# Performance work log

Hardware: AMD Instinct MI355X
Metric: run time of the kernel (lower is better)

## Reference

```python
import jax, jax.numpy as jnp
import numpy as np

B, H, W, D = 32, 56, 56, 192
WS, NH, SHIFT = 7, 6, 3
DH = D // NH          # head dim = 32
N = WS * WS           # 49 tokens per window
NW = (H // WS) * (W // WS)  # 64 windows per image
EPS = 1e-5


def _rel_pos_index():
    coords = np.stack(np.meshgrid(np.arange(WS), np.arange(WS), indexing='ij'))  # (2,WS,WS)
    flat = coords.reshape(2, -1)
    rel = flat[:, :, None] - flat[:, None, :]            # (2,N,N)
    rel = rel.transpose(1, 2, 0).astype(np.int64)        # (N,N,2)
    rel[..., 0] += WS - 1
    rel[..., 1] += WS - 1
    rel[..., 0] *= 2 * WS - 1
    return rel.sum(-1)                                    # (N,N) in [0,169)


def _shift_mask():
    img = np.zeros((H, W))
    bounds = [(0, H - WS), (H - WS, H - SHIFT), (H - SHIFT, H)]
    cnt = 0
    for h0, h1 in bounds:
        for w0, w1 in bounds:
            img[h0:h1, w0:w1] = cnt
            cnt += 1
    win = img.reshape(H // WS, WS, W // WS, WS).transpose(0, 2, 1, 3).reshape(-1, N)  # (nW,N)
    diff = win[:, None, :] - win[:, :, None]
    return np.where(diff != 0, -100.0, 0.0).astype(np.float32)  # (nW,N,N)


_REL_IDX = jnp.asarray(_rel_pos_index())
_MASK = jnp.asarray(_shift_mask())


def _layernorm(x, g, b):
    mu = jnp.mean(x, -1, keepdims=True)
    var = jnp.mean(jnp.square(x - mu), -1, keepdims=True)
    return (x - mu) * jax.lax.rsqrt(var + EPS) * g + b


def _window_partition(x):  # (B,H,W,C) -> (B*nW, N, C)
    Bx, _, _, C = x.shape
    x = x.reshape(Bx, H // WS, WS, W // WS, WS, C).transpose(0, 1, 3, 2, 4, 5)
    return x.reshape(-1, N, C)


def _window_reverse(w):  # (B*nW, N, C) -> (B,H,W,C)
    C = w.shape[-1]
    x = w.reshape(-1, H // WS, W // WS, WS, WS, C).transpose(0, 1, 3, 2, 4, 5)
    return x.reshape(-1, H, W, C)


def setup_inputs() -> dict:
    key = jax.random.key(0)
    ks = jax.random.split(key, 8)
    s = 0.02
    return {
        'x': jax.random.normal(ks[0], (B, H * W, D), jnp.float32),
        'norm1_g': jnp.ones((D,), jnp.float32),
        'norm1_b': jnp.zeros((D,), jnp.float32),
        'qkv_w': jax.random.normal(ks[1], (D, 3 * D), jnp.float32) * s,
        'qkv_b': jnp.zeros((3 * D,), jnp.float32),
        'proj_wo': jax.random.normal(ks[2], (D, D), jnp.float32) * s,
        'proj_bo': jnp.zeros((D,), jnp.float32),
        'rpb': jax.random.normal(ks[3], ((2 * WS - 1) ** 2, NH), jnp.float32) * s,
        'pl_w': jax.random.normal(ks[4], (NH, NH), jnp.float32) * s,
        'pl_b': jnp.zeros((NH,), jnp.float32),
        'pw_w': jax.random.normal(ks[5], (NH, NH), jnp.float32) * s,
        'pw_b': jnp.zeros((NH,), jnp.float32),
        'norm2_g': jnp.ones((D,), jnp.float32),
        'norm2_b': jnp.zeros((D,), jnp.float32),
        'fc1_w': jax.random.normal(ks[6], (D, 4 * D), jnp.float32) * s,
        'fc1_b': jnp.zeros((4 * D,), jnp.float32),
        'fc2_w': jax.random.normal(ks[7], (4 * D, D), jnp.float32) * s,
        'fc2_b': jnp.zeros((D,), jnp.float32),
    }


def reference(x, norm1_g, norm1_b, qkv_w, qkv_b, proj_wo, proj_bo, rpb,
              pl_w, pl_b, pw_w, pw_b, norm2_g, norm2_b,
              fc1_w, fc1_b, fc2_w, fc2_b):
    shortcut = x
    h = _layernorm(x, norm1_g, norm1_b).reshape(B, H, W, D)
    h = jnp.roll(h, (-SHIFT, -SHIFT), (1, 2))             # shifted windows
    win = _window_partition(h)                            # (B_, N, D), B_ = B*NW
    B_ = win.shape[0]

    qkv = win @ qkv_w + qkv_b                             # (B_, N, 3D)
    q_out, k_out, v_out = qkv[..., :D], qkv[..., D:2 * D], qkv[..., 2 * D:]
    qkv5 = qkv.reshape(B_, N, 3, NH, DH)
    q = qkv5[:, :, 0].transpose(0, 2, 1, 3)               # (B_, H, N, d)
    k = qkv5[:, :, 1].transpose(0, 2, 1, 3)
    v = qkv5[:, :, 2].transpose(0, 2, 1, 3)

    scale = DH ** -0.5
    attn = jnp.einsum('bhnd,bhmd->bhnm', q * scale, k)    # (B_, H, N, N)
    bias = rpb[_REL_IDX.reshape(-1)].reshape(N, N, NH).transpose(2, 0, 1)
    attn = attn + bias[None]
    # proj_l over the head axis (distillation transform, pre-softmax)
    attn = jnp.einsum('bhnm,hg->bgnm', attn, pl_w) + pl_b[None, :, None, None]
    # shifted-window mask
    attn = attn.reshape(B, NW, NH, N, N) + _MASK[None, :, None]
    attn = jax.nn.softmax(attn.reshape(B_, NH, N, N), axis=-1)
    # proj_w over the head axis (post-softmax)
    attn = jnp.einsum('bhnm,hg->bgnm', attn, pw_w) + pw_b[None, :, None, None]

    out = jnp.einsum('bhnm,bhmd->bnhd', attn, v).reshape(B_, N, D)
    out = out @ proj_wo + proj_bo

    h = _window_reverse(out)                              # (B,H,W,D)
    h = jnp.roll(h, (SHIFT, SHIFT), (1, 2)).reshape(B, H * W, D)
    xo = shortcut + h

    m = _layernorm(xo, norm2_g, norm2_b)
    m = jax.nn.gelu(m @ fc1_w + fc1_b, approximate=False) @ fc2_w + fc2_b
    xo = xo + m
    return xo, (q_out, k_out, v_out)
```

## Files before the change

### kernel.cpp

```cpp
#include <hip/hip_runtime.h>
#include <math.h>

#define TOK   100352
#define OUTCH 19267584L
#define NWIN  2048

typedef __attribute__((ext_vector_type(4))) float f32x4;
typedef __attribute__((ext_vector_type(8))) short bf16x8;

__device__ __forceinline__ unsigned short f2bf(float f) {
    unsigned u = __builtin_bit_cast(unsigned, f);
    u += 0x7FFFu + ((u >> 16) & 1u);
    return (unsigned short)(u >> 16);
}
__device__ __forceinline__ float bf2f(unsigned short s) {
    return __builtin_bit_cast(float, (unsigned)s << 16);
}

__global__ __launch_bounds__(256) void k_prep_w(const float* __restrict__ qkv_w,
                                                const float* __restrict__ proj_w,
                                                const float* __restrict__ fc1_w,
                                                const float* __restrict__ fc2_w,
                                                unsigned short* __restrict__ wt)
{
    int i = blockIdx.x * 256 + threadIdx.x;
    float v;
    if (i < 110592) {
        int instr = i >> 9, rem = i & 511, lane = rem >> 3, j = rem & 7;
        int ks = instr % 6, t = instr / 6;
        int ni = t % 3, t2 = t / 3;
        int wv = t2 & 3, s = t2 >> 2;
        int n = s * 192 + wv * 48 + ni * 16 + (lane & 15);
        int k = ks * 32 + ((lane >> 4) << 3) + j;
        v = qkv_w[k * 576 + n];
    } else if (i < 147456) {
        int j2 = i - 110592;
        int instr = j2 >> 9, rem = j2 & 511, lane = rem >> 3, j = rem & 7;
        int ks = instr % 6, t = instr / 6;
        int ni = t % 3, wv = t / 3;
        int n = wv * 48 + ni * 16 + (lane & 15);
        int k = ks * 32 + ((lane >> 4) << 3) + j;
        v = proj_w[k * 192 + n];
    } else if (i < 294912) {
        int j2 = i - 147456;
        int instr = j2 >> 9, rem = j2 & 511, lane = rem >> 3, j = rem & 7;
        int ks = instr % 6, t = instr / 6;
        int ni = t % 3, t2 = t / 3;
        int wv = t2 & 3, s = t2 >> 2;
        int n = s * 192 + wv * 48 + ni * 16 + (lane & 15);
        int k = ks * 32 + ((lane >> 4) << 3) + j;
        v = fc1_w[k * 768 + n];
    } else {
        int j2 = i - 294912;
        int instr = j2 >> 9, rem = j2 & 511, lane = rem >> 3, j = rem & 7;
        int ks = instr % 6, t = instr / 6;
        int ni = t % 3, t2 = t / 3;
        int wv = t2 & 3, s = t2 >> 2;
        int n = wv * 48 + ni * 16 + (lane & 15);
        int k = s * 192 + ks * 32 + ((lane >> 4) << 3) + j;
        v = fc2_w[k * 192 + n];
    }
    wt[i] = f2bf(v);
}

__global__ __launch_bounds__(256) void k_qkv(const float* __restrict__ x,
                                             const float* __restrict__ g,
                                             const float* __restrict__ b,
                                             const unsigned short* __restrict__ wp,
                                             const float* __restrict__ bias,
                                             float* __restrict__ outq)
{
    __shared__ unsigned short lA[64 * 192];
    const int tid = threadIdx.x, lane = tid & 63, wv = tid >> 6;
    const int s = blockIdx.x;
    const long m0 = (long)blockIdx.y * 64;

    {
        int r = tid >> 2, c0 = (tid & 3) * 48;
        int t = (int)m0 + r;
        int w = t / 49, n = t - w * 49;
        int bb = w >> 6, widx = w & 63;
        int wi = widx >> 3, wj = widx & 7;
        int rr = n / 7, ss = n - rr * 7;
        int hh = wi * 7 + rr + 3; if (hh >= 56) hh -= 56;
        int ww = wj * 7 + ss + 3; if (ww >= 56) ww -= 56;
        const f32x4* sp = (const f32x4*)(x + ((long)(bb * 56 + hh) * 56 + ww) * 192 + c0);
        f32x4 vv[12];
        float sum = 0.f, sq = 0.f;
        #pragma unroll
        for (int i = 0; i < 12; i++) {
            vv[i] = sp[i];
            #pragma unroll
            for (int j = 0; j < 4; j++) { sum += vv[i][j]; sq += vv[i][j] * vv[i][j]; }
        }
        sum += __shfl_xor(sum, 1); sq += __shfl_xor(sq, 1);
        sum += __shfl_xor(sum, 2); sq += __shfl_xor(sq, 2);
        float mu = sum * (1.f / 192.f);
        float rs = rsqrtf(sq * (1.f / 192.f) - mu * mu + 1e-5f);
        #pragma unroll
        for (int i = 0; i < 6; i++) {
            bf16x8 o8;
            #pragma unroll
            for (int j = 0; j < 8; j++) {
                int idx = i * 8 + j, c = c0 + idx;
                o8[j] = (short)f2bf((vv[idx >> 2][idx & 3] - mu) * rs * g[c] + b[c]);
            }
            *(bf16x8*)((char*)lA + r * 384 + ((2 * (c0 + i * 8)) ^ ((r & 7) << 4))) = o8;
        }
    }
    __syncthreads();

    f32x4 acc[4][3];
    #pragma unroll
    for (int mi = 0; mi < 4; mi++)
        #pragma unroll
        for (int ni = 0; ni < 3; ni++) acc[mi][ni] = (f32x4){0.f, 0.f, 0.f, 0.f};
    #pragma unroll
    for (int ks = 0; ks < 6; ks++) {
        int kb = ks * 64 + ((lane >> 4) << 4);
        bf16x8 bfr[3];
        #pragma unroll
        for (int ni = 0; ni < 3; ni++) {
            int instr = ((s * 4 + wv) * 3 + ni) * 6 + ks;
            bfr[ni] = *(const bf16x8*)(wp + (instr << 9) + (lane << 3));
        }
        #pragma unroll
        for (int mi = 0; mi < 4; mi++) {
            int row = mi * 16 + (lane & 15);
            bf16x8 afr = *(const bf16x8*)((char*)lA + row * 384 + (kb ^ ((row & 7) << 4)));
            #pragma unroll
            for (int ni = 0; ni < 3; ni++)
                acc[mi][ni] = __builtin_amdgcn_mfma_f32_16x16x32_bf16(afr, bfr[ni], acc[mi][ni], 0, 0, 0);
        }
    }

    #pragma unroll
    for (int mi = 0; mi < 4; mi++)
        #pragma unroll
        for (int ni = 0; ni < 3; ni++) {
            int gc = wv * 48 + ni * 16 + (lane & 15);
            float bv = bias[s * 192 + gc];
            #pragma unroll
            for (int r4 = 0; r4 < 4; r4++) {
                long lr = mi * 16 + ((lane >> 4) << 2) + r4;
                outq[(long)s * OUTCH + (m0 + lr) * 192 + gc] = acc[mi][ni][r4] + bv;
            }
        }
}

__global__ __launch_bounds__(256) void k_proj(const unsigned short* __restrict__ aspat,
                                              const unsigned short* __restrict__ wp,
                                              const float* __restrict__ pbias,
                                              const float* __restrict__ x,
                                              const float* __restrict__ g2,
                                              const float* __restrict__ b2,
                                              unsigned short* __restrict__ xv,
                                              unsigned short* __restrict__ h2)
{
    __shared__ unsigned short lA[64 * 192];
    __shared__ float xoT[64][196];
    const int tid = threadIdx.x, lane = tid & 63, wv = tid >> 6;
    const long m0 = (long)blockIdx.x * 64;

    #pragma unroll
    for (int c = tid; c < 64 * 24; c += 256) {
        int row = c / 24, k16 = c - row * 24;
        bf16x8 v = *(const bf16x8*)(aspat + (m0 + row) * 192 + k16 * 8);
        *(bf16x8*)((char*)lA + row * 384 + ((k16 * 16) ^ ((row & 7) << 4))) = v;
    }
    __syncthreads();

    f32x4 acc[4][3];
    #pragma unroll
    for (int mi = 0; mi < 4; mi++)
        #pragma unroll
        for (int ni = 0; ni < 3; ni++) acc[mi][ni] = (f32x4){0.f, 0.f, 0.f, 0.f};
    #pragma unroll
    for (int ks = 0; ks < 6; ks++) {
        int kb = ks * 64 + ((lane >> 4) << 4);
        bf16x8 bfr[3];
        #pragma unroll
        for (int ni = 0; ni < 3; ni++) {
            int instr = (wv * 3 + ni) * 6 + ks;
            bfr[ni] = *(const bf16x8*)(wp + (instr << 9) + (lane << 3));
        }
        #pragma unroll
        for (int mi = 0; mi < 4; mi++) {
            int row = mi * 16 + (lane & 15);
            bf16x8 afr = *(const bf16x8*)((char*)lA + row * 384 + (kb ^ ((row & 7) << 4)));
            #pragma unroll
            for (int ni = 0; ni < 3; ni++)
                acc[mi][ni] = __builtin_amdgcn_mfma_f32_16x16x32_bf16(afr, bfr[ni], acc[mi][ni], 0, 0, 0);
        }
    }

    #pragma unroll
    for (int mi = 0; mi < 4; mi++)
        #pragma unroll
        for (int ni = 0; ni < 3; ni++) {
            int gc = wv * 48 + ni * 16 + (lane & 15);
            float bv = pbias[gc];
            #pragma unroll
            for (int r4 = 0; r4 < 4; r4++) {
                int lr = mi * 16 + ((lane >> 4) << 2) + r4;
                xoT[lr][gc] = x[(m0 + lr) * 192 + gc] + acc[mi][ni][r4] + bv;
            }
        }
    __syncthreads();

    {
        int r = tid >> 2, c0 = (tid & 3) * 48;
        float vv[48];
        float sum = 0.f, sq = 0.f;
        #pragma unroll
        for (int i = 0; i < 48; i++) { vv[i] = xoT[r][c0 + i]; sum += vv[i]; sq += vv[i] * vv[i]; }
        sum += __shfl_xor(sum, 1); sq += __shfl_xor(sq, 1);
        sum += __shfl_xor(sum, 2); sq += __shfl_xor(sq, 2);
        float mu = sum * (1.f / 192.f);
        float rs = rsqrtf(sq * (1.f / 192.f) - mu * mu + 1e-5f);
        #pragma unroll
        for (int i = 0; i < 6; i++) {
            bf16x8 o8, x8;
            #pragma unroll
            for (int j = 0; j < 8; j++) {
                int c = c0 + i * 8 + j;
                float xvf = vv[i * 8 + j];
                x8[j] = (short)f2bf(xvf);
                o8[j] = (short)f2bf((xvf - mu) * rs * g2[c] + b2[c]);
            }
            *(bf16x8*)(h2 + (m0 + r) * 192 + c0 + i * 8) = o8;
            *(bf16x8*)(xv + (m0 + r) * 192 + c0 + i * 8) = x8;
        }
    }
}

__global__ __launch_bounds__(256) void k_mlp(const unsigned short* __restrict__ h2,
                                             const unsigned short* __restrict__ w1p,
                                             const float* __restrict__ b1,
                                             const unsigned short* __restrict__ w2p,
                                             const float* __restrict__ b2,
                                             const unsigned short* __restrict__ xv,
                                             float* __restrict__ xo)
{
    __shared__ unsigned short lA[64 * 192];
    __shared__ unsigned short lH[64 * 192];
    const int tid = threadIdx.x, lane = tid & 63, wv = tid >> 6;
    const long m0 = (long)blockIdx.x * 64;

    #pragma unroll
    for (int c = tid; c < 64 * 24; c += 256) {
        int row = c / 24, k16 = c - row * 24;
        bf16x8 v = *(const bf16x8*)(h2 + (m0 + row) * 192 + k16 * 8);
        *(bf16x8*)((char*)lA + row * 384 + ((k16 * 16) ^ ((row & 7) << 4))) = v;
    }

    f32x4 acc2[4][3];
    #pragma unroll
    for (int mi = 0; mi < 4; mi++)
        #pragma unroll
        for (int ni = 0; ni < 3; ni++) acc2[mi][ni] = (f32x4){0.f, 0.f, 0.f, 0.f};
    __syncthreads();

    for (int s = 0; s < 4; s++) {
        f32x4 acc1[4][3];
        #pragma unroll
        for (int mi = 0; mi < 4; mi++)
            #pragma unroll
            for (int ni = 0; ni < 3; ni++) acc1[mi][ni] = (f32x4){0.f, 0.f, 0.f, 0.f};
        #pragma unroll
        for (int ks = 0; ks < 6; ks++) {
            int kb = ks * 64 + ((lane >> 4) << 4);
            bf16x8 bfr[3];
            #pragma unroll
            for (int ni = 0; ni < 3; ni++) {
                int instr = ((s * 4 + wv) * 3 + ni) * 6 + ks;
                bfr[ni] = *(const bf16x8*)(w1p + (instr << 9) + (lane << 3));
            }
            #pragma unroll
            for (int mi = 0; mi < 4; mi++) {
                int row = mi * 16 + (lane & 15);
                bf16x8 afr = *(const bf16x8*)((char*)lA + row * 384 + (kb ^ ((row & 7) << 4)));
                #pragma unroll
                for (int ni = 0; ni < 3; ni++)
                    acc1[mi][ni] = __builtin_amdgcn_mfma_f32_16x16x32_bf16(afr, bfr[ni], acc1[mi][ni], 0, 0, 0);
            }
        }
        __syncthreads();
        #pragma unroll
        for (int mi = 0; mi < 4; mi++)
            #pragma unroll
            for (int ni = 0; ni < 3; ni++) {
                int col = wv * 48 + ni * 16 + (lane & 15);
                float bv = b1[s * 192 + col];
                #pragma unroll
                for (int r = 0; r < 4; r++) {
                    int row = mi * 16 + ((lane >> 4) << 2) + r;
                    float v = acc1[mi][ni][r] + bv;
                    float ge = 0.5f * v * (1.f + erff(v * 0.70710678118654752f));
                    *(unsigned short*)((char*)lH + row * 384 + ((2 * col) ^ ((row & 7) << 4))) = f2bf(ge);
                }
            }
        __syncthreads();
        #pragma unroll
        for (int ks = 0; ks < 6; ks++) {
            int kb = ks * 64 + ((lane >> 4) << 4);
            bf16x8 bfr[3];
            #pragma unroll
            for (int ni = 0; ni < 3; ni++) {
                int instr = ((s * 4 + wv) * 3 + ni) * 6 + ks;
                bfr[ni] = *(const bf16x8*)(w2p + (instr << 9) + (lane << 3));
            }
            #pragma unroll
            for (int mi = 0; mi < 4; mi++) {
                int row = mi * 16 + (lane & 15);
                bf16x8 afr = *(const bf16x8*)((char*)lH + row * 384 + (kb ^ ((row & 7) << 4)));
                #pragma unroll
                for (int ni = 0; ni < 3; ni++)
                    acc2[mi][ni] = __builtin_amdgcn_mfma_f32_16x16x32_bf16(afr, bfr[ni], acc2[mi][ni], 0, 0, 0);
            }
        }
    }
    #pragma unroll
    for (int mi = 0; mi < 4; mi++)
        #pragma unroll
        for (int ni = 0; ni < 3; ni++) {
            int gcol = wv * 48 + ni * 16 + (lane & 15);
            float bv = b2[gcol];
            #pragma unroll
            for (int r = 0; r < 4; r++) {
                long grow = m0 + mi * 16 + ((lane >> 4) << 2) + r;
                xo[grow * 192 + gcol] = bf2f(xv[grow * 192 + gcol]) + acc2[mi][ni][r] + bv;
            }
        }
}

#define ATS 67
__global__ __launch_bounds__(384) void k_attn(const float* __restrict__ qg,
                                              const float* __restrict__ kg,
                                              const float* __restrict__ vg,
                                              const float* __restrict__ rpb,
                                              const float* __restrict__ plw,
                                              const float* __restrict__ plb,
                                              const float* __restrict__ pww,
                                              const float* __restrict__ pwb,
                                              unsigned short* __restrict__ aout)
{
    __shared__ float ATT[6][49][ATS];

    int w = blockIdx.x, widx = w & 63;
    int tid = threadIdx.x, lane = tid & 63, h = tid >> 6;
    const long base = (long)w * 49 * 192;

    bf16x8 vfr[2][2];
    #pragma unroll
    for (int kst = 0; kst < 2; kst++)
        #pragma unroll
        for (int ni = 0; ni < 2; ni++) {
            int d = ni * 16 + (lane & 15);
            #pragma unroll
            for (int j = 0; j < 8; j++) {
                int n = kst * 32 + ((lane >> 4) << 3) + j; if (n > 48) n = 48;
                vfr[kst][ni][j] = (short)f2bf(vg[base + n * 192 + h * 32 + d]);
            }
        }

    for (int c = tid; c < 6 * 49 * 15; c += 384) {
        int g2 = c / (49 * 15), rem = c - g2 * (49 * 15);
        int m = rem / 15, n = 49 + (rem - m * 15);
        ATT[g2][m][n] = 0.f;
    }

    bf16x8 qfr[4], kfr[4];
    #pragma unroll
    for (int mi = 0; mi < 4; mi++) {
        int m = mi * 16 + (lane & 15); if (m > 48) m = 48;
        const float* qp = qg + base + m * 192 + h * 32 + ((lane >> 4) << 3);
        #pragma unroll
        for (int j = 0; j < 8; j++) qfr[mi][j] = (short)f2bf(qp[j]);
    }
    #pragma unroll
    for (int ni = 0; ni < 4; ni++) {
        int n = ni * 16 + (lane & 15); if (n > 48) n = 48;
        const float* kp = kg + base + n * 192 + h * 32 + ((lane >> 4) << 3);
        #pragma unroll
        for (int j = 0; j < 8; j++) kfr[ni][j] = (short)f2bf(kp[j]);
    }
    f32x4 sa[4][4];
    #pragma unroll
    for (int ni = 0; ni < 4; ni++)
        #pragma unroll
        for (int mi = 0; mi < 4; mi++)
            sa[mi][ni] = __builtin_amdgcn_mfma_f32_16x16x32_bf16(qfr[mi], kfr[ni], (f32x4){0.f, 0.f, 0.f, 0.f}, 0, 0, 0);
    const float scale = 0.17677669529663687f;
    #pragma unroll
    for (int mi = 0; mi < 4; mi++)
        #pragma unroll
        for (int ni = 0; ni < 4; ni++)
            #pragma unroll
            for (int r = 0; r < 4; r++) {
                int m = mi * 16 + ((lane >> 4) << 2) + r, n = ni * 16 + (lane & 15);
                if (m < 49 && n < 49) {
                    int rq = m / 7, cq = m - rq * 7, rk = n / 7, ck = n - rk * 7;
                    int ridx = (rq - rk + 6) * 13 + (cq - ck + 6);
                    ATT[h][m][n] = sa[mi][ni][r] * scale + rpb[ridx * 6 + h];
                }
            }
    __syncthreads();

    int wi = widx >> 3, wj = widx & 7;
    for (int p = tid; p < 2401; p += 384) {
        int m = p / 49, n = p - m * 49;
        float a[6];
        #pragma unroll
        for (int g2 = 0; g2 < 6; g2++) a[g2] = ATT[g2][m][n];
        int rq = m / 7, cq = m - rq * 7, rk = n / 7, ck = n - rk * 7;
        int ghq = wi * 7 + rq, gwq = wj * 7 + cq, ghk = wi * 7 + rk, gwk = wj * 7 + ck;
        int regq = (ghq < 49 ? 0 : (ghq < 53 ? 1 : 2)) * 3 + (gwq < 49 ? 0 : (gwq < 53 ? 1 : 2));
        int regk = (ghk < 49 ? 0 : (ghk < 53 ? 1 : 2)) * 3 + (gwk < 49 ? 0 : (gwk < 53 ? 1 : 2));
        float msk = (regq != regk) ? -100.f : 0.f;
        #pragma unroll
        for (int g2 = 0; g2 < 6; g2++) {
            float v = plb[g2] + msk;
            #pragma unroll
            for (int h2 = 0; h2 < 6; h2++) v += a[h2] * plw[h2 * 6 + g2];
            ATT[g2][m][n] = v;
        }
    }
    __syncthreads();

    if (tid < 294) {
        int g2 = tid / 49, m = tid - g2 * 49;
        float* row = &ATT[g2][m][0];
        float mx = row[0];
        #pragma unroll
        for (int j = 1; j < 49; j++) mx = fmaxf(mx, row[j]);
        float e[49]; float sm = 0.f;
        #pragma unroll
        for (int j = 0; j < 49; j++) { e[j] = __expf(row[j] - mx); sm += e[j]; }
        float inv = 1.f / sm;
        #pragma unroll
        for (int j = 0; j < 49; j++) row[j] = e[j] * inv;
    }
    __syncthreads();

    for (int p = tid; p < 2401; p += 384) {
        int m = p / 49, n = p - m * 49;
        float a[6];
        #pragma unroll
        for (int g2 = 0; g2 < 6; g2++) a[g2] = ATT[g2][m][n];
        #pragma unroll
        for (int g2 = 0; g2 < 6; g2++) {
            float v = pwb[g2];
            #pragma unroll
            for (int h2 = 0; h2 < 6; h2++) v += a[h2] * pww[h2 * 6 + g2];
            ATT[g2][m][n] = v;
        }
    }
    __syncthreads();

    f32x4 oa[4][2];
    #pragma unroll
    for (int mi = 0; mi < 4; mi++)
        #pragma unroll
        for (int ni = 0; ni < 2; ni++) oa[mi][ni] = (f32x4){0.f, 0.f, 0.f, 0.f};
    #pragma unroll
    for (int kst = 0; kst < 2; kst++) {
        #pragma unroll
        for (int mi = 0; mi < 4; mi++) {
            int m = mi * 16 + (lane & 15); if (m > 48) m = 48;
            const float* ap = &ATT[h][m][kst * 32 + ((lane >> 4) << 3)];
            bf16x8 afr;
            #pragma unroll
            for (int j = 0; j < 8; j++) afr[j] = (short)f2bf(ap[j]);
            #pragma unroll
            for (int ni = 0; ni < 2; ni++)
                oa[mi][ni] = __builtin_amdgcn_mfma_f32_16x16x32_bf16(afr, vfr[kst][ni], oa[mi][ni], 0, 0, 0);
        }
    }
    int bb = w >> 6;
    #pragma unroll
    for (int mi = 0; mi < 4; mi++)
        #pragma unroll
        for (int ni = 0; ni < 2; ni++)
            #pragma unroll
            for (int r = 0; r < 4; r++) {
                int m = mi * 16 + ((lane >> 4) << 2) + r, d = ni * 16 + (lane & 15);
                if (m < 49) {
                    int rr = m / 7, ss = m - rr * 7;
                    int ho = wi * 7 + rr + 3; if (ho >= 56) ho -= 56;
                    int wo = wj * 7 + ss + 3; if (wo >= 56) wo -= 56;
                    long tp = ((long)(bb * 56 + ho) * 56 + wo);
                    aout[tp * 192 + h * 32 + d] = f2bf(oa[mi][ni][r]);
                }
            }
}

extern "C" void kernel_launch(void* const* d_in, const int* in_sizes, int n_in,
                              void* d_out, int out_size, void* d_ws, size_t ws_size,
                              hipStream_t stream)
{
    const float* x      = (const float*)d_in[0];
    const float* n1g    = (const float*)d_in[1];
    const float* n1b    = (const float*)d_in[2];
    const float* qkv_w  = (const float*)d_in[3];
    const float* qkv_b  = (const float*)d_in[4];
    const float* proj_w = (const float*)d_in[5];
    const float* proj_b = (const float*)d_in[6];
    const float* rpb    = (const float*)d_in[7];
    const float* pl_w   = (const float*)d_in[8];
    const float* pl_b   = (const float*)d_in[9];
    const float* pw_w   = (const float*)d_in[10];
    const float* pw_b   = (const float*)d_in[11];
    const float* n2g    = (const float*)d_in[12];
    const float* n2b    = (const float*)d_in[13];
    const float* fc1_w  = (const float*)d_in[14];
    const float* fc1_b  = (const float*)d_in[15];
    const float* fc2_w  = (const float*)d_in[16];
    const float* fc2_b  = (const float*)d_in[17];

    float* out   = (float*)d_out;
    float* out_q = out + OUTCH;
    float* out_k = out + 2 * OUTCH;
    float* out_v = out + 3 * OUTCH;

    char* ws = (char*)d_ws;
    unsigned short* bufT = (unsigned short*)ws;
    unsigned short* xvB  = (unsigned short*)(ws + 38535168);
    unsigned short* bufW = (unsigned short*)(ws + 2 * 38535168L);

    k_prep_w<<<1728, 256, 0, stream>>>(qkv_w, proj_w, fc1_w, fc2_w, bufW);
    k_qkv<<<dim3(3, 1568), 256, 0, stream>>>(x, n1g, n1b, bufW, qkv_b, out_q);
    k_attn<<<NWIN, 384, 0, stream>>>(out_q, out_k, out_v,
                                     rpb, pl_w, pl_b, pw_w, pw_b, bufT);
    k_proj<<<1568, 256, 0, stream>>>(bufT, bufW + 110592, proj_b, x, n2g, n2b,
                                     xvB, bufT);
    k_mlp<<<1568, 256, 0, stream>>>(bufT, bufW + 147456, fc1_b, bufW + 294912, fc2_b,
                                    xvB, out);
}
```

Before: 458.3 us.

## Fuse output projection, residual and LayerNorm2 into windowed attention kernel

Removes the separate k_proj kernel and performs the output projection, residual add and second LayerNorm inside k_attn, per window, using shared memory for the attention output tile. The proj weight pre-pack is reorganized to per-head 32-column slices to match the six-wave attention block. This drops a bf16 round trip of the attention output through global memory and one kernel launch. In exchange shared memory per block rises to about 79KB, which can lower occupancy, and the 49-row window pads the MFMA work for the projection.

Measured after the change: 459.7 us. No clear change (+0.3%).

```diff
diff --git a/kernel.cpp b/kernel.cpp
--- a/kernel.cpp
+++ b/kernel.cpp
@@ -37,8 +37,8 @@
         int j2 = i - 110592;
         int instr = j2 >> 9, rem = j2 & 511, lane = rem >> 3, j = rem & 7;
         int ks = instr % 6, t = instr / 6;
-        int ni = t % 3, wv = t / 3;
-        int n = wv * 48 + ni * 16 + (lane & 15);
+        int ni = t & 1, hh = t >> 1;
+        int n = hh * 32 + ni * 16 + (lane & 15);
         int k = ks * 32 + ((lane >> 4) << 3) + j;
         v = proj_w[k * 192 + n];
     } else if (i < 294912) {
@@ -148,92 +148,6 @@
         }
 }
 
-__global__ __launch_bounds__(256) void k_proj(const unsigned short* __restrict__ aspat,
-                                              const unsigned short* __restrict__ wp,
-                                              const float* __restrict__ pbias,
-                                              const float* __restrict__ x,
-                                              const float* __restrict__ g2,
-                                              const float* __restrict__ b2,
-                                              unsigned short* __restrict__ xv,
-                                              unsigned short* __restrict__ h2)
-{
-    __shared__ unsigned short lA[64 * 192];
-    __shared__ float xoT[64][196];
-    const int tid = threadIdx.x, lane = tid & 63, wv = tid >> 6;
-    const long m0 = (long)blockIdx.x * 64;
-
-    #pragma unroll
-    for (int c = tid; c < 64 * 24; c += 256) {
-        int row = c / 24, k16 = c - row * 24;
-        bf16x8 v = *(const bf16x8*)(aspat + (m0 + row) * 192 + k16 * 8);
-        *(bf16x8*)((char*)lA + row * 384 + ((k16 * 16) ^ ((row & 7) << 4))) = v;
-    }
-    __syncthreads();
-
-    f32x4 acc[4][3];
-    #pragma unroll
-    for (int mi = 0; mi < 4; mi++)
-        #pragma unroll
-        for (int ni = 0; ni < 3; ni++) acc[mi][ni] = (f32x4){0.f, 0.f, 0.f, 0.f};
-    #pragma unroll
-    for (int ks = 0; ks < 6; ks++) {
-        int kb = ks * 64 + ((lane >> 4) << 4);
-        bf16x8 bfr[3];
-        #pragma unroll
-        for (int ni = 0; ni < 3; ni++) {
-            int instr = (wv * 3 + ni) * 6 + ks;
-            bfr[ni] = *(const bf16x8*)(wp + (instr << 9) + (lane << 3));
-        }
-        #pragma unroll
-        for (int mi = 0; mi < 4; mi++) {
-            int row = mi * 16 + (lane & 15);
-            bf16x8 afr = *(const bf16x8*)((char*)lA + row * 384 + (kb ^ ((row & 7) << 4)));
-            #pragma unroll
-            for (int ni = 0; ni < 3; ni++)
-                acc[mi][ni] = __builtin_amdgcn_mfma_f32_16x16x32_bf16(afr, bfr[ni], acc[mi][ni], 0, 0, 0);
-        }
-    }
-
-    #pragma unroll
-    for (int mi = 0; mi < 4; mi++)
-        #pragma unroll
-        for (int ni = 0; ni < 3; ni++) {
-            int gc = wv * 48 + ni * 16 + (lane & 15);
-            float bv = pbias[gc];
-            #pragma unroll
-            for (int r4 = 0; r4 < 4; r4++) {
-                int lr = mi * 16 + ((lane >> 4) << 2) + r4;
-                xoT[lr][gc] = x[(m0 + lr) * 192 + gc] + acc[mi][ni][r4] + bv;
-            }
-        }
-    __syncthreads();
-
-    {
-        int r = tid >> 2, c0 = (tid & 3) * 48;
-        float vv[48];
-        float sum = 0.f, sq = 0.f;
-        #pragma unroll
-        for (int i = 0; i < 48; i++) { vv[i] = xoT[r][c0 + i]; sum += vv[i]; sq += vv[i] * vv[i]; }
-        sum += __shfl_xor(sum, 1); sq += __shfl_xor(sq, 1);
-        sum += __shfl_xor(sum, 2); sq += __shfl_xor(sq, 2);
-        float mu = sum * (1.f / 192.f);
-        float rs = rsqrtf(sq * (1.f / 192.f) - mu * mu + 1e-5f);
-        #pragma unroll
-        for (int i = 0; i < 6; i++) {
-            bf16x8 o8, x8;
-            #pragma unroll
-            for (int j = 0; j < 8; j++) {
-                int c = c0 + i * 8 + j;
-                float xvf = vv[i * 8 + j];
-                x8[j] = (short)f2bf(xvf);
-                o8[j] = (short)f2bf((xvf - mu) * rs * g2[c] + b2[c]);
-            }
-            *(bf16x8*)(h2 + (m0 + r) * 192 + c0 + i * 8) = o8;
-            *(bf16x8*)(xv + (m0 + r) * 192 + c0 + i * 8) = x8;
-        }
-    }
-}
-
 __global__ __launch_bounds__(256) void k_mlp(const unsigned short* __restrict__ h2,
                                              const unsigned short* __restrict__ w1p,
                                              const float* __restrict__ b1,
@@ -343,13 +257,22 @@
                                               const float* __restrict__ plb,
                                               const float* __restrict__ pww,
                                               const float* __restrict__ pwb,
-                                              unsigned short* __restrict__ aout)
+                                              const unsigned short* __restrict__ projp,
+                                              const float* __restrict__ pbias,
+                                              const float* __restrict__ x,
+                                              const float* __restrict__ g2,
+                                              const float* __restrict__ b2,
+                                              unsigned short* __restrict__ xv,
+                                              unsigned short* __restrict__ h2)
 {
-    __shared__ float ATT[6][49][ATS];
+    __shared__ __align__(16) char SM[78800];
+    float (*ATT)[49][ATS] = (float(*)[49][ATS])SM;
+    float (*xoT)[196]     = (float(*)[196])(SM + 19200);
 
     int w = blockIdx.x, widx = w & 63;
     int tid = threadIdx.x, lane = tid & 63, h = tid >> 6;
     const long base = (long)w * 49 * 192;
+    int wi = widx >> 3, wj = widx & 7, bb = w >> 6;
 
     bf16x8 vfr[2][2];
     #pragma unroll
@@ -365,9 +288,9 @@
         }
 
     for (int c = tid; c < 6 * 49 * 15; c += 384) {
-        int g2 = c / (49 * 15), rem = c - g2 * (49 * 15);
+        int g = c / (49 * 15), rem = c - g * (49 * 15);
         int m = rem / 15, n = 49 + (rem - m * 15);
-        ATT[g2][m][n] = 0.f;
+        ATT[g][m][n] = 0.f;
     }
 
     bf16x8 qfr[4], kfr[4];
@@ -407,30 +330,29 @@
             }
     __syncthreads();
 
-    int wi = widx >> 3, wj = widx & 7;
     for (int p = tid; p < 2401; p += 384) {
         int m = p / 49, n = p - m * 49;
         float a[6];
         #pragma unroll
-        for (int g2 = 0; g2 < 6; g2++) a[g2] = ATT[g2][m][n];
+        for (int g = 0; g < 6; g++) a[g] = ATT[g][m][n];
         int rq = m / 7, cq = m - rq * 7, rk = n / 7, ck = n - rk * 7;
         int ghq = wi * 7 + rq, gwq = wj * 7 + cq, ghk = wi * 7 + rk, gwk = wj * 7 + ck;
         int regq = (ghq < 49 ? 0 : (ghq < 53 ? 1 : 2)) * 3 + (gwq < 49 ? 0 : (gwq < 53 ? 1 : 2));
         int regk = (ghk < 49 ? 0 : (ghk < 53 ? 1 : 2)) * 3 + (gwk < 49 ? 0 : (gwk < 53 ? 1 : 2));
         float msk = (regq != regk) ? -100.f : 0.f;
         #pragma unroll
-        for (int g2 = 0; g2 < 6; g2++) {
-            float v = plb[g2] + msk;
-            #pragma unroll
-            for (int h2 = 0; h2 < 6; h2++) v += a[h2] * plw[h2 * 6 + g2];
-            ATT[g2][m][n] = v;
+        for (int g = 0; g < 6; g++) {
+            float v = plb[g] + msk;
+            #pragma unroll
+            for (int h2i = 0; h2i < 6; h2i++) v += a[h2i] * plw[h2i * 6 + g];
+            ATT[g][m][n] = v;
         }
     }
     __syncthreads();
 
     if (tid < 294) {
-        int g2 = tid / 49, m = tid - g2 * 49;
-        float* row = &ATT[g2][m][0];
+        int g = tid / 49, m = tid - g * 49;
+        float* row = &ATT[g][m][0];
         float mx = row[0];
         #pragma unroll
         for (int j = 1; j < 49; j++) mx = fmaxf(mx, row[j]);
@@ -447,13 +369,13 @@
         int m = p / 49, n = p - m * 49;
         float a[6];
         #pragma unroll
-        for (int g2 = 0; g2 < 6; g2++) a[g2] = ATT[g2][m][n];
-        #pragma unroll
-        for (int g2 = 0; g2 < 6; g2++) {
-            float v = pwb[g2];
-            #pragma unroll
-            for (int h2 = 0; h2 < 6; h2++) v += a[h2] * pww[h2 * 6 + g2];
-            ATT[g2][m][n] = v;
+        for (int g = 0; g < 6; g++) a[g] = ATT[g][m][n];
+        #pragma unroll
+        for (int g = 0; g < 6; g++) {
+            float v = pwb[g];
+            #pragma unroll
+            for (int h2i = 0; h2i < 6; h2i++) v += a[h2i] * pww[h2i * 6 + g];
+            ATT[g][m][n] = v;
         }
     }
     __syncthreads();
@@ -477,22 +399,94 @@
                 oa[mi][ni] = __builtin_amdgcn_mfma_f32_16x16x32_bf16(afr, vfr[kst][ni], oa[mi][ni], 0, 0, 0);
         }
     }
-    int bb = w >> 6;
+    __syncthreads();
+
     #pragma unroll
     for (int mi = 0; mi < 4; mi++)
         #pragma unroll
         for (int ni = 0; ni < 2; ni++)
             #pragma unroll
             for (int r = 0; r < 4; r++) {
-                int m = mi * 16 + ((lane >> 4) << 2) + r, d = ni * 16 + (lane & 15);
+                int m = mi * 16 + ((lane >> 4) << 2) + r;
+                if (m < 49) {
+                    int col = h * 32 + ni * 16 + (lane & 15);
+                    *(unsigned short*)(SM + m * 384 + ((2 * col) ^ ((m & 7) << 4))) = f2bf(oa[mi][ni][r]);
+                }
+            }
+    __syncthreads();
+
+    f32x4 pacc[4][2];
+    #pragma unroll
+    for (int mi = 0; mi < 4; mi++)
+        #pragma unroll
+        for (int ni = 0; ni < 2; ni++) pacc[mi][ni] = (f32x4){0.f, 0.f, 0.f, 0.f};
+    #pragma unroll
+    for (int ks = 0; ks < 6; ks++) {
+        int kb = ks * 64 + ((lane >> 4) << 4);
+        bf16x8 bfr[2];
+        #pragma unroll
+        for (int ni = 0; ni < 2; ni++) {
+            int instr = (h * 2 + ni) * 6 + ks;
+            bfr[ni] = *(const bf16x8*)(projp + (instr << 9) + (lane << 3));
+        }
+        #pragma unroll
+        for (int mi = 0; mi < 4; mi++) {
+            int row = mi * 16 + (lane & 15); if (row > 48) row = 48;
+            bf16x8 afr = *(const bf16x8*)(SM + row * 384 + (kb ^ ((row & 7) << 4)));
+            #pragma unroll
+            for (int ni = 0; ni < 2; ni++)
+                pacc[mi][ni] = __builtin_amdgcn_mfma_f32_16x16x32_bf16(afr, bfr[ni], pacc[mi][ni], 0, 0, 0);
+        }
+    }
+
+    #pragma unroll
+    for (int mi = 0; mi < 4; mi++)
+        #pragma unroll
+        for (int ni = 0; ni < 2; ni++) {
+            int gc = h * 32 + ni * 16 + (lane & 15);
+            float bv = pbias[gc];
+            #pragma unroll
+            for (int r = 0; r < 4; r++) {
+                int m = mi * 16 + ((lane >> 4) << 2) + r;
                 if (m < 49) {
                     int rr = m / 7, ss = m - rr * 7;
                     int ho = wi * 7 + rr + 3; if (ho >= 56) ho -= 56;
                     int wo = wj * 7 + ss + 3; if (wo >= 56) wo -= 56;
                     long tp = ((long)(bb * 56 + ho) * 56 + wo);
-                    aout[tp * 192 + h * 32 + d] = f2bf(oa[mi][ni][r]);
+                    xoT[m][gc] = x[tp * 192 + gc] + pacc[mi][ni][r] + bv;
                 }
             }
+        }
+    __syncthreads();
+
+    if (tid < 196) {
+        int m = tid >> 2, c0 = (tid & 3) * 48;
+        float vv[48];
+        float sum = 0.f, sq = 0.f;
+        #pragma unroll
+        for (int i = 0; i < 48; i++) { vv[i] = xoT[m][c0 + i]; sum += vv[i]; sq += vv[i] * vv[i]; }
+        sum += __shfl_xor(sum, 1); sq += __shfl_xor(sq, 1);
+        sum += __shfl_xor(sum, 2); sq += __shfl_xor(sq, 2);
+        float mu = sum * (1.f / 192.f);
+        float rs = rsqrtf(sq * (1.f / 192.f) - mu * mu + 1e-5f);
+        int rr = m / 7, ss = m - rr * 7;
+        int ho = wi * 7 + rr + 3; if (ho >= 56) ho -= 56;
+        int wo = wj * 7 + ss + 3; if (wo >= 56) wo -= 56;
+        long tp = ((long)(bb * 56 + ho) * 56 + wo);
+        #pragma unroll
+        for (int i = 0; i < 6; i++) {
+            bf16x8 o8, x8;
+            #pragma unroll
+            for (int j = 0; j < 8; j++) {
+                int c = c0 + i * 8 + j;
+                float xvf = vv[i * 8 + j];
+                x8[j] = (short)f2bf(xvf);
+                o8[j] = (short)f2bf((xvf - mu) * rs * g2[c] + b2[c]);
+            }
+            *(bf16x8*)(h2 + tp * 192 + c0 + i * 8) = o8;
+            *(bf16x8*)(xv + tp * 192 + c0 + i * 8) = x8;
+        }
+    }
 }
 
 extern "C" void kernel_launch(void* const* d_in, const int* in_sizes, int n_in,
@@ -531,8 +525,8 @@
     k_prep_w<<<1728, 256, 0, stream>>>(qkv_w, proj_w, fc1_w, fc2_w, bufW);
     k_qkv<<<dim3(3, 1568), 256, 0, stream>>>(x, n1g, n1b, bufW, qkv_b, out_q);
     k_attn<<<NWIN, 384, 0, stream>>>(out_q, out_k, out_v,
-                                     rpb, pl_w, pl_b, pw_w, pw_b, bufT);
-    k_proj<<<1568, 256, 0, stream>>>(bufT, bufW + 110592, proj_b, x, n2g, n2b,
+                                     rpb, pl_w, pl_b, pw_w, pw_b,
+                                     bufW + 110592, proj_b, x, n2g, n2b,
                                      xvB, bufT);
     k_mlp<<<1568, 256, 0, stream>>>(bufT, bufW + 147456, fc1_b, bufW + 294912, fc2_b,
                                     xvB, out);
```
